# Kernel tuning notes

Measured on AMD Instinct MI355X. Metric: run time of the kernel, lower is better.

Reference implementation:

```python
import jax, jax.numpy as jnp
import numpy as np
from jax import lax

B, N, M = 4, 16384, 2048
C_IN = 64
RADII = (0.2, 0.4)
KS = (32, 64)
MLPS = ((64, 64, 128), (64, 96, 128))
EPS = 1e-5


def setup_inputs() -> dict:
    key = jax.random.key(0)
    ks = jax.random.split(key, 32)
    inp = {}
    inp["xyz"] = jax.random.uniform(ks[0], (B, 3, N), jnp.float32)
    inp["feature"] = jax.random.normal(ks[1], (B, C_IN, N), jnp.float32)
    ki = 2
    for s, chans in enumerate(MLPS):
        cin = C_IN + 3  # use_xyz concatenates relative xyz
        for l, cout in enumerate(chans):
            inp[f"w{s}{l}"] = jax.random.normal(ks[ki], (cout, cin), jnp.float32) * (1.0 / np.sqrt(cin)); ki += 1
            inp[f"g{s}{l}"] = jnp.ones((cout,), jnp.float32)
            inp[f"b{s}{l}"] = jnp.zeros((cout,), jnp.float32)
            cin = cout
    return inp


def _fps(points):
    """Farthest point sampling. points [N,3] -> [M] int32 indices (starts at 0)."""
    n = points.shape[0]
    def step(carry, _):
        dists, last = carry
        d = jnp.sum((points - points[last]) ** 2, axis=-1)
        dists = jnp.minimum(dists, d)
        nxt = jnp.argmax(dists).astype(jnp.int32)
        return (dists, nxt), nxt
    init = (jnp.full((n,), 1e10, jnp.float32), jnp.int32(0))
    _, rest = lax.scan(step, init, None, length=M - 1)
    return jnp.concatenate([jnp.zeros((1,), jnp.int32), rest])


def _ball_query(xyz, new_xyz, radius, k):
    """xyz [B,3,N], new_xyz [B,3,M] -> [B,M,k] int32. First-found semantics: empty
    slots are filled with the first valid index (pointnet2 ball_query behavior)."""
    xyz = lax.stop_gradient(xyz)
    new_xyz = lax.stop_gradient(new_xyz)
    n = xyz.shape[-1]
    sq_x = jnp.sum(xyz ** 2, axis=1)          # [B,N]
    sq_c = jnp.sum(new_xyz ** 2, axis=1)      # [B,M]
    d2 = sq_c[:, :, None] + sq_x[:, None, :] - 2.0 * jnp.einsum('bdm,bdn->bmn', new_xyz, xyz)
    scores = jnp.where(d2 < radius * radius, jnp.arange(n, dtype=jnp.int32), n)
    idx = -lax.top_k(-scores, k)[0]           # k smallest indices (in order)
    first = idx[..., :1]
    idx = jnp.where(idx >= n, first, idx)
    return jnp.where(idx >= n, 0, idx)


def _group(feat, idx):
    """feat [B,C,N], idx [B,M,K] -> [B,C,M,K]"""
    return jax.vmap(lambda f, i: f[:, i])(feat, idx)


def _forward(xyz, feature, params):
    idx = jax.vmap(_fps)(jnp.transpose(lax.stop_gradient(xyz), (0, 2, 1)))  # [B,M]
    new_xyz = jnp.take_along_axis(xyz, idx[:, None, :].astype(jnp.int32), axis=2)  # [B,3,M]
    feats = []
    for s in range(len(MLPS)):
        nidx = _ball_query(xyz, new_xyz, RADII[s], KS[s])        # [B,M,K]
        gxyz = _group(xyz, nidx) - new_xyz[..., None]            # [B,3,M,K]
        x = jnp.concatenate([gxyz, _group(feature, nidx)], axis=1)  # [B,3+C,M,K]
        for l in range(len(MLPS[s])):
            w = params[f"w{s}{l}"]; g = params[f"g{s}{l}"]; b = params[f"b{s}{l}"]
            x = jnp.einsum('oc,bcmk->bomk', w, x)                # 1x1 conv
            mu = jnp.mean(x, axis=(0, 2, 3), keepdims=True)      # train-mode BN
            var = jnp.mean((x - mu) ** 2, axis=(0, 2, 3), keepdims=True)
            x = (x - mu) * lax.rsqrt(var + EPS)
            x = x * g[None, :, None, None] + b[None, :, None, None]
            x = jax.nn.relu(x)
        feats.append(jnp.max(x, axis=3))                         # max over neighbors
    return new_xyz, jnp.concatenate(feats, axis=1)               # [B,3,M], [B,256,M]


def reference(xyz, feature, w00, g00, b00, w01, g01, b01, w02, g02, b02,
              w10, g10, b10, w11, g11, b11, w12, g12, b12):
    params = dict(w00=w00, g00=g00, b00=b00, w01=w01, g01=g01, b01=b01,
                  w02=w02, g02=g02, b02=b02, w10=w10, g10=g10, b10=b10,
                  w11=w11, g11=g11, b11=b11, w12=w12, g12=g12, b12=b12)
    return _forward(xyz, feature, params)
```

## Files before the change

kernel.cpp:

```cpp
#include <hip/hip_runtime.h>
#include <cstdint>

constexpr int B_ = 4, N_ = 16384, M_ = 2048;
constexpr int COLS0 = B_ * M_ * 32;
constexpr int COLS1 = B_ * M_ * 64;

constexpr int FPS_G   = 8;
constexpr int FPS_T   = 512;
constexpr int FPS_PPT = N_ / FPS_G / FPS_T;

constexpr size_t OFF_NEWXYZ = 0;
constexpr size_t OFF_NIDX0  = (size_t)B_ * 3 * M_ * 4;
constexpr size_t OFF_NIDX1  = OFF_NIDX0 + (size_t)COLS0 * 4;
constexpr size_t OFF_STATS  = OFF_NIDX1 + (size_t)COLS1 * 4;
constexpr size_t STATS_VALS = 64 * 2 * 128;
constexpr size_t OFF_COEF   = OFF_STATS + 6 * STATS_VALS * 8;
constexpr size_t OFF_SLOT   = OFF_COEF + 6 * 128 * 16;
constexpr size_t SLOT_BYTES = (size_t)B_ * 2 * FPS_G * 64;
constexpr size_t OFF_Z      = OFF_SLOT + SLOT_BYTES;
constexpr int ZSTRIDE = 96 * 64;

__global__ __launch_bounds__(FPS_T) void fps_kernel(const float* __restrict__ xyz,
                                                    float* __restrict__ newxyz,
                                                    float* __restrict__ outxyz,
                                                    unsigned long long* __restrict__ slots) {
#pragma clang fp contract(off)
  int bid = blockIdx.x;
  int b = bid >> 3, g = bid & 7;
  int t = threadIdx.x, lane = t & 63, wid = t >> 6;
  const float* xb = xyz + (size_t)b * 3 * N_;
  int nbase = g * (N_ / FPS_G) + t;
  float px[FPS_PPT], py[FPS_PPT], pz[FPS_PPT], dd[FPS_PPT];
#pragma unroll
  for (int j = 0; j < FPS_PPT; ++j) {
    int n = nbase + j * FPS_T;
    px[j] = xb[n]; py[j] = xb[N_ + n]; pz[j] = xb[2 * N_ + n];
    dd[j] = 1e10f;
    asm volatile("" : "+v"(px[j]), "+v"(py[j]), "+v"(pz[j]));
  }
  __shared__ unsigned long long s_red[2][FPS_T / 64];
  __shared__ unsigned long long s_win[2];
  size_t base = (size_t)b * 3 * M_;
  float fx = xb[0], fy = xb[N_], fz = xb[2 * N_];
  if (g == 0 && t == 0) {
    newxyz[base] = fx; newxyz[base + M_] = fy; newxyz[base + 2 * M_] = fz;
    outxyz[base] = fx; outxyz[base + M_] = fy; outxyz[base + 2 * M_] = fz;
  }
  unsigned long long* sb = slots + (size_t)b * 2 * FPS_G * 8;
  for (int s = 1; s < M_; ++s) {
    float bv = -1.f; int bi = 0;
#pragma unroll
    for (int j = 0; j < FPS_PPT; ++j) {
      float dx = px[j] - fx, dy = py[j] - fy, dz = pz[j] - fz;
      float d = (dx * dx + dy * dy) + dz * dz;
      float dm = dd[j];
      if (d < dm) dm = d;
      dd[j] = dm;
      if (dm > bv) { bv = dm; bi = nbase + j * FPS_T; }
    }
    unsigned long long key =
        ((unsigned long long)__float_as_uint(bv) << 32) |
        (unsigned)(((unsigned)s << 14) | (unsigned)(0x3FFF - bi));
#pragma unroll
    for (int off = 1; off < 64; off <<= 1) {
      unsigned long long o = __shfl_xor(key, off);
      if (o > key) key = o;
    }
    int p = s & 1;
    if (lane == 0) s_red[p][wid] = key;
    __syncthreads();
    if (wid == 0) {
      unsigned long long bk = s_red[p][lane & 7];
#pragma unroll
      for (int off = 1; off < 8; off <<= 1) {
        unsigned long long o = __shfl_xor(bk, off);
        if (o > bk) bk = o;
      }
      unsigned long long kk = 0;
      if (lane < FPS_G) {
        unsigned long long* sp = sb + ((size_t)p * FPS_G + lane) * 8;
        if (lane == g) atomicExch(sp, bk);
        unsigned long long v;
        unsigned tag = (unsigned)s;
        for (int it = 0; it < (1 << 18); ++it) {
          v = atomicAdd(sp, 0ull);
          if ((unsigned)((v >> 14) & 0x3FFFFull) == tag) break;
          __builtin_amdgcn_s_sleep(1);
        }
        kk = v;
      }
#pragma unroll
      for (int off = 1; off < 8; off <<= 1) {
        unsigned long long o = __shfl_xor(kk, off);
        if (o > kk) kk = o;
      }
      if (lane == 0) s_win[p] = kk;
    }
    __syncthreads();
    unsigned long long k = s_win[p];
    int w = 0x3FFF - (int)(k & 0x3FFFull);
    fx = xb[w]; fy = xb[N_ + w]; fz = xb[2 * N_ + w];
    if (g == 0 && t == 0) {
      newxyz[base + s] = fx; newxyz[base + M_ + s] = fy; newxyz[base + 2 * M_ + s] = fz;
      outxyz[base + s] = fx; outxyz[base + M_ + s] = fy; outxyz[base + 2 * M_ + s] = fz;
    }
  }
}

template <int KNB>
__global__ __launch_bounds__(256) void bq_kernel(const float* __restrict__ xyz,
                                                 const float* __restrict__ newxyz,
                                                 int* __restrict__ nidx, float r2) {
#pragma clang fp contract(off)
  int t = threadIdx.x, lane = t & 63, wq = t >> 6;
  int q = blockIdx.x * 4 + wq;
  int b = q >> 11, m = q & 2047;
  const float* xb = xyz + (size_t)b * 3 * N_;
  float cx = newxyz[((size_t)b * 3 + 0) * M_ + m];
  float cy = newxyz[((size_t)b * 3 + 1) * M_ + m];
  float cz = newxyz[((size_t)b * 3 + 2) * M_ + m];
  float sqc = (cx * cx + cy * cy) + cz * cz;
  int found = 0, first = 0;
  for (int c = 0; c < N_ / 64; ++c) {
    int n = c * 64 + lane;
    float x = xb[n], y = xb[N_ + n], z = xb[2 * N_ + n];
    float sqx = (x * x + y * y) + z * z;
    float dot = fmaf(cz, z, fmaf(cy, y, cx * x));
    float d2 = (sqc + sqx) - 2.0f * dot;
    bool in = d2 < r2;
    unsigned long long mask = __ballot(in);
    if (mask) {
      if (found == 0) first = c * 64 + (__ffsll((long long)mask) - 1);
      int pos = found + __popcll(mask & ((1ull << lane) - 1ull));
      if (in && pos < KNB) nidx[(size_t)q * KNB + pos] = n;
      found += __popcll(mask);
      if (found >= KNB) break;
    }
  }
  if (found < KNB) {
    int fill = (found == 0) ? 0 : first;
    for (int s = found + lane; s < KNB; s += 64) nidx[(size_t)q * KNB + s] = fill;
  }
}

__device__ __forceinline__ void stat_accum(float acc, int o, int cout, double* stats,
                                           int part, int lane) {
  float v1 = acc, v2 = acc * acc;
#pragma unroll
  for (int off = 1; off < 64; off <<= 1) {
    v1 += __shfl_xor(v1, off);
    v2 += __shfl_xor(v2, off);
  }
  if (lane == 0) {
    atomicAdd(stats + ((size_t)part * 2 + 0) * cout + o, (double)v1);
    atomicAdd(stats + ((size_t)part * 2 + 1) * cout + o, (double)v2);
  }
}

template <int KNB>
__global__ __launch_bounds__(256) void convL0_kernel(
    const float* __restrict__ w0,
    const float* __restrict__ xyz, const float* __restrict__ feat,
    const int* __restrict__ nidx, const float* __restrict__ newxyz,
    float* __restrict__ Z, double* __restrict__ stats) {
  int lane = threadIdx.x & 63, wq = threadIdx.x >> 6;
  int rec = blockIdx.x * 4 + wq;
  int col = rec * 64 + lane;
  float x[67];
  {
    int b = col / (M_ * KNB);
    int rem = col - b * (M_ * KNB);
    int m = rem / KNB;
    int n = nidx[col];
    const float* xb = xyz + (size_t)b * 3 * N_;
    x[0] = xb[n]          - newxyz[((size_t)b * 3 + 0) * M_ + m];
    x[1] = xb[N_ + n]     - newxyz[((size_t)b * 3 + 1) * M_ + m];
    x[2] = xb[2 * N_ + n] - newxyz[((size_t)b * 3 + 2) * M_ + m];
    const float* fb = feat + (size_t)b * 64 * N_;
#pragma unroll
    for (int c = 0; c < 64; ++c) x[3 + c] = fb[(size_t)c * N_ + n];
  }
  float* zr = Z + (size_t)rec * ZSTRIDE;
  int part = rec & 63;
  for (int o = 0; o < 64; ++o) {
    const float* wr = w0 + (size_t)o * 67;
    float acc = 0.f;
#pragma unroll
    for (int c = 0; c < 67; ++c) acc += wr[c] * x[c];
    zr[o * 64 + lane] = acc;
    stat_accum(acc, o, 64, stats, part, lane);
  }
}

template <int CIN, int COUT>
__global__ __launch_bounds__(256) void convMid_kernel(
    const float* __restrict__ w,
    const float4* __restrict__ coefIn,
    float* __restrict__ Z, double* __restrict__ stats) {
  int lane = threadIdx.x & 63, wq = threadIdx.x >> 6;
  int rec = blockIdx.x * 4 + wq;
  float* zr = Z + (size_t)rec * ZSTRIDE;
  float x[CIN];
#pragma unroll
  for (int c = 0; c < CIN; ++c) {
    float v = zr[c * 64 + lane];
    float4 cf = coefIn[c];
    x[c] = fmaxf(((v - cf.x) * cf.y) * cf.z + cf.w, 0.f);
  }
  int part = rec & 63;
  for (int o = 0; o < COUT; ++o) {
    const float* wr = w + (size_t)o * CIN;
    float acc = 0.f;
#pragma unroll
    for (int c = 0; c < CIN; ++c) acc += wr[c] * x[c];
    zr[o * 64 + lane] = acc;
    stat_accum(acc, o, COUT, stats, part, lane);
  }
}

template <int CIN>
__global__ __launch_bounds__(256) void convLastStats_kernel(
    const float* __restrict__ w, const float4* __restrict__ coefIn,
    const float* __restrict__ Z, double* __restrict__ stats) {
  int lane = threadIdx.x & 63, wq = threadIdx.x >> 6;
  int rec = blockIdx.x * 4 + wq;
  const float* zr = Z + (size_t)rec * ZSTRIDE;
  float x[CIN];
#pragma unroll
  for (int c = 0; c < CIN; ++c) {
    float v = zr[c * 64 + lane];
    float4 cf = coefIn[c];
    x[c] = fmaxf(((v - cf.x) * cf.y) * cf.z + cf.w, 0.f);
  }
  int part = rec & 63;
  for (int o = 0; o < 128; ++o) {
    const float* wr = w + (size_t)o * CIN;
    float acc = 0.f;
#pragma unroll
    for (int c = 0; c < CIN; ++c) acc += wr[c] * x[c];
    stat_accum(acc, o, 128, stats, part, lane);
  }
}

template <int CIN, int KNB>
__global__ __launch_bounds__(256) void convLastPool_kernel(
    const float* __restrict__ w, const float4* __restrict__ coefIn,
    const float4* __restrict__ coefOut,
    const float* __restrict__ Z, float* __restrict__ outFeats, int chBase) {
  int lane = threadIdx.x & 63, wq = threadIdx.x >> 6;
  int rec = blockIdx.x * 4 + wq;
  const float* zr = Z + (size_t)rec * ZSTRIDE;
  float x[CIN];
#pragma unroll
  for (int c = 0; c < CIN; ++c) {
    float v = zr[c * 64 + lane];
    float4 cf = coefIn[c];
    x[c] = fmaxf(((v - cf.x) * cf.y) * cf.z + cf.w, 0.f);
  }
  for (int o = 0; o < 128; ++o) {
    const float* wr = w + (size_t)o * CIN;
    float acc = 0.f;
#pragma unroll
    for (int c = 0; c < CIN; ++c) acc += wr[c] * x[c];
    float4 cf = coefOut[o];
    float z = fmaxf(((acc - cf.x) * cf.y) * cf.z + cf.w, 0.f);
    if (KNB == 64) {
#pragma unroll
      for (int off = 1; off < 64; off <<= 1) z = fmaxf(z, __shfl_xor(z, off));
      if (lane == 0) {
        int b = rec >> 11, m = rec & 2047;
        outFeats[((size_t)b * 256 + chBase + o) * M_ + m] = z;
      }
    } else {
#pragma unroll
      for (int off = 1; off < 32; off <<= 1) z = fmaxf(z, __shfl_xor(z, off));
      if ((lane & 31) == 0) {
        int grp = rec * 2 + (lane >> 5);
        int b = grp >> 11, m = grp & 2047;
        outFeats[((size_t)b * 256 + chBase + o) * M_ + m] = z;
      }
    }
  }
}

__global__ void coef_kernel(const double* __restrict__ stats, const float* __restrict__ g,
                            const float* __restrict__ bb, float4* __restrict__ coef,
                            int cout, double invcnt) {
  int ch = threadIdx.x;
  if (ch >= cout) return;
  double s1 = 0.0, s2 = 0.0;
  for (int p = 0; p < 64; ++p) {
    s1 += stats[((size_t)p * 2 + 0) * cout + ch];
    s2 += stats[((size_t)p * 2 + 1) * cout + ch];
  }
  double mean = s1 * invcnt;
  double var = s2 * invcnt - mean * mean;
  double rstd = 1.0 / sqrt(var + 1e-5);
  coef[ch] = make_float4((float)mean, (float)rstd, g[ch], bb[ch]);
}

extern "C" void kernel_launch(void* const* d_in, const int* in_sizes, int n_in,
                              void* d_out, int out_size, void* d_ws, size_t ws_size,
                              hipStream_t stream) {
  const float* xyz  = (const float*)d_in[0];
  const float* feat = (const float*)d_in[1];
  const float* w00 = (const float*)d_in[2],  *g00 = (const float*)d_in[3],  *b00 = (const float*)d_in[4];
  const float* w01 = (const float*)d_in[5],  *g01 = (const float*)d_in[6],  *b01 = (const float*)d_in[7];
  const float* w02 = (const float*)d_in[8],  *g02 = (const float*)d_in[9],  *b02 = (const float*)d_in[10];
  const float* w10 = (const float*)d_in[11], *g10 = (const float*)d_in[12], *b10 = (const float*)d_in[13];
  const float* w11 = (const float*)d_in[14], *g11 = (const float*)d_in[15], *b11 = (const float*)d_in[16];
  const float* w12 = (const float*)d_in[17], *g12 = (const float*)d_in[18], *b12 = (const float*)d_in[19];

  char* ws = (char*)d_ws;
  float*  newxyz = (float*)(ws + OFF_NEWXYZ);
  int*    nidx0  = (int*)(ws + OFF_NIDX0);
  int*    nidx1  = (int*)(ws + OFF_NIDX1);
  double* stats  = (double*)(ws + OFF_STATS);
  float4* coef   = (float4*)(ws + OFF_COEF);
  unsigned long long* slots = (unsigned long long*)(ws + OFF_SLOT);
  float*  Z      = (float*)(ws + OFF_Z);
  float* outF = (float*)d_out;
  float* outFeats = outF + (size_t)B_ * 3 * M_;

  hipMemsetAsync(ws + OFF_STATS, 0, 6 * STATS_VALS * 8, stream);
  hipMemsetAsync(ws + OFF_SLOT, 0, SLOT_BYTES, stream);
  fps_kernel<<<B_ * FPS_G, FPS_T, 0, stream>>>(xyz, newxyz, outF, slots);
  bq_kernel<32><<<(B_ * M_) / 4, 256, 0, stream>>>(xyz, newxyz, nidx0, (float)(0.2 * 0.2));
  bq_kernel<64><<<(B_ * M_) / 4, 256, 0, stream>>>(xyz, newxyz, nidx1, (float)(0.4 * 0.4));

  float4* c00 = coef + 0 * 128; float4* c01 = coef + 1 * 128; float4* c02 = coef + 2 * 128;
  float4* c10 = coef + 3 * 128; float4* c11 = coef + 4 * 128; float4* c12 = coef + 5 * 128;
  double* st0 = stats + 0 * STATS_VALS; double* st1 = stats + 1 * STATS_VALS;
  double* st2 = stats + 2 * STATS_VALS; double* st3 = stats + 3 * STATS_VALS;
  double* st4 = stats + 4 * STATS_VALS; double* st5 = stats + 5 * STATS_VALS;
  int gb0 = (COLS0 / 64) / 4, gb1 = (COLS1 / 64) / 4;

  convL0_kernel<32><<<gb0, 256, 0, stream>>>(w00, xyz, feat, nidx0, newxyz, Z, st0);
  coef_kernel<<<1, 128, 0, stream>>>(st0, g00, b00, c00, 64, 1.0 / COLS0);
  convMid_kernel<64, 64><<<gb0, 256, 0, stream>>>(w01, c00, Z, st1);
  coef_kernel<<<1, 128, 0, stream>>>(st1, g01, b01, c01, 64, 1.0 / COLS0);
  convLastStats_kernel<64><<<gb0, 256, 0, stream>>>(w02, c01, Z, st2);
  coef_kernel<<<1, 128, 0, stream>>>(st2, g02, b02, c02, 128, 1.0 / COLS0);
  convLastPool_kernel<64, 32><<<gb0, 256, 0, stream>>>(w02, c01, c02, Z, outFeats, 0);

  convL0_kernel<64><<<gb1, 256, 0, stream>>>(w10, xyz, feat, nidx1, newxyz, Z, st3);
  coef_kernel<<<1, 128, 0, stream>>>(st3, g10, b10, c10, 64, 1.0 / COLS1);
  convMid_kernel<64, 96><<<gb1, 256, 0, stream>>>(w11, c10, Z, st4);
  coef_kernel<<<1, 128, 0, stream>>>(st4, g11, b11, c11, 96, 1.0 / COLS1);
  convLastStats_kernel<96><<<gb1, 256, 0, stream>>>(w12, c11, Z, st5);
  coef_kernel<<<1, 128, 0, stream>>>(st5, g12, b12, c12, 128, 1.0 / COLS1);
  convLastPool_kernel<96, 64><<<gb1, 256, 0, stream>>>(w12, c11, c12, Z, outFeats, 128);
}
```

Measured before the change: 5.473 ms.

## Stage 64-column activation tiles in LDS and split output channels across waves

Each block now handles a single 64-column record. It stages the BN-ReLU'd input activations (or the gathered features for layer 0) into shared memory once. The four waves then split the output channels, each computing 8 channels at a time from the shared tile. This replaces the previous scheme where each wave held all CIN inputs in registers and swept every output channel serially. The goal is lower register pressure, higher occupancy and more ILP per wave, at the cost of LDS traffic, an extra barrier, and 4x more blocks.

```diff
diff --git a/kernel.cpp b/kernel.cpp
--- a/kernel.cpp
+++ b/kernel.cpp
@@ -157,64 +157,98 @@
   }
 }
 
+template <int CIN, int G>
+__device__ __forceinline__ void conv_sweep(const float* __restrict__ w, int o0,
+                                           const float* sx, int lane, float* acc) {
+#pragma unroll
+  for (int k = 0; k < G; ++k) acc[k] = 0.f;
+#pragma unroll 16
+  for (int c = 0; c < CIN; ++c) {
+    float xv = sx[c * 64 + lane];
+#pragma unroll
+    for (int k = 0; k < G; ++k) acc[k] += w[(size_t)(o0 + 4 * k) * CIN + c] * xv;
+  }
+}
+
+template <int CIN>
+__device__ __forceinline__ void stage_bn(const float* __restrict__ zr,
+                                         const float4* __restrict__ coefIn,
+                                         float* sx, int t) {
+  const float4* zr4 = (const float4*)zr;
+  float4* sx4 = (float4*)sx;
+  for (int e = t; e < CIN * 16; e += 256) {
+    int c = e >> 4;
+    float4 v = zr4[e];
+    float4 cf = coefIn[c];
+    float4 r;
+    r.x = fmaxf(((v.x - cf.x) * cf.y) * cf.z + cf.w, 0.f);
+    r.y = fmaxf(((v.y - cf.x) * cf.y) * cf.z + cf.w, 0.f);
+    r.z = fmaxf(((v.z - cf.x) * cf.y) * cf.z + cf.w, 0.f);
+    r.w = fmaxf(((v.w - cf.x) * cf.y) * cf.z + cf.w, 0.f);
+    sx4[e] = r;
+  }
+}
+
 template <int KNB>
 __global__ __launch_bounds__(256) void convL0_kernel(
-    const float* __restrict__ w0,
-    const float* __restrict__ xyz, const float* __restrict__ feat,
-    const int* __restrict__ nidx, const float* __restrict__ newxyz,
-    float* __restrict__ Z, double* __restrict__ stats) {
-  int lane = threadIdx.x & 63, wq = threadIdx.x >> 6;
-  int rec = blockIdx.x * 4 + wq;
-  int col = rec * 64 + lane;
-  float x[67];
-  {
+    const float* __restrict__ w0, const float* __restrict__ xyz,
+    const float* __restrict__ feat, const int* __restrict__ nidx,
+    const float* __restrict__ newxyz, float* __restrict__ Z, double* __restrict__ stats) {
+  __shared__ float sx[67 * 64];
+  __shared__ int snb[64];
+  int rec = blockIdx.x, t = threadIdx.x, lane = t & 63, wid = t >> 6;
+  if (t < 64) snb[t] = nidx[(size_t)rec * 64 + t];
+  __syncthreads();
+  for (int e = t; e < 67 * 64; e += 256) {
+    int c = e >> 6, l = e & 63;
+    int col = rec * 64 + l;
     int b = col / (M_ * KNB);
     int rem = col - b * (M_ * KNB);
     int m = rem / KNB;
-    int n = nidx[col];
-    const float* xb = xyz + (size_t)b * 3 * N_;
-    x[0] = xb[n]          - newxyz[((size_t)b * 3 + 0) * M_ + m];
-    x[1] = xb[N_ + n]     - newxyz[((size_t)b * 3 + 1) * M_ + m];
-    x[2] = xb[2 * N_ + n] - newxyz[((size_t)b * 3 + 2) * M_ + m];
-    const float* fb = feat + (size_t)b * 64 * N_;
-#pragma unroll
-    for (int c = 0; c < 64; ++c) x[3 + c] = fb[(size_t)c * N_ + n];
-  }
+    int n = snb[l];
+    float v;
+    if (c < 3) v = xyz[((size_t)b * 3 + c) * N_ + n] - newxyz[((size_t)b * 3 + c) * M_ + m];
+    else       v = feat[((size_t)b * 64 + (c - 3)) * N_ + n];
+    sx[e] = v;
+  }
+  __syncthreads();
   float* zr = Z + (size_t)rec * ZSTRIDE;
   int part = rec & 63;
-  for (int o = 0; o < 64; ++o) {
-    const float* wr = w0 + (size_t)o * 67;
-    float acc = 0.f;
-#pragma unroll
-    for (int c = 0; c < 67; ++c) acc += wr[c] * x[c];
-    zr[o * 64 + lane] = acc;
-    stat_accum(acc, o, 64, stats, part, lane);
+  float acc[8];
+#pragma unroll
+  for (int g = 0; g < 2; ++g) {
+    int o0 = wid + 32 * g;
+    conv_sweep<67, 8>(w0, o0, sx, lane, acc);
+#pragma unroll
+    for (int k = 0; k < 8; ++k) {
+      int o = o0 + 4 * k;
+      zr[o * 64 + lane] = acc[k];
+      stat_accum(acc[k], o, 64, stats, part, lane);
+    }
   }
 }
 
 template <int CIN, int COUT>
 __global__ __launch_bounds__(256) void convMid_kernel(
-    const float* __restrict__ w,
-    const float4* __restrict__ coefIn,
+    const float* __restrict__ w, const float4* __restrict__ coefIn,
     float* __restrict__ Z, double* __restrict__ stats) {
-  int lane = threadIdx.x & 63, wq = threadIdx.x >> 6;
-  int rec = blockIdx.x * 4 + wq;
+  __shared__ float sx[CIN * 64];
+  int rec = blockIdx.x, t = threadIdx.x, lane = t & 63, wid = t >> 6;
   float* zr = Z + (size_t)rec * ZSTRIDE;
-  float x[CIN];
-#pragma unroll
-  for (int c = 0; c < CIN; ++c) {
-    float v = zr[c * 64 + lane];
-    float4 cf = coefIn[c];
-    x[c] = fmaxf(((v - cf.x) * cf.y) * cf.z + cf.w, 0.f);
-  }
+  stage_bn<CIN>(zr, coefIn, sx, t);
+  __syncthreads();
   int part = rec & 63;
-  for (int o = 0; o < COUT; ++o) {
-    const float* wr = w + (size_t)o * CIN;
-    float acc = 0.f;
-#pragma unroll
-    for (int c = 0; c < CIN; ++c) acc += wr[c] * x[c];
-    zr[o * 64 + lane] = acc;
-    stat_accum(acc, o, COUT, stats, part, lane);
+  float acc[8];
+#pragma unroll
+  for (int g = 0; g < COUT / 32; ++g) {
+    int o0 = wid + 32 * g;
+    conv_sweep<CIN, 8>(w, o0, sx, lane, acc);
+#pragma unroll
+    for (int k = 0; k < 8; ++k) {
+      int o = o0 + 4 * k;
+      zr[o * 64 + lane] = acc[k];
+      stat_accum(acc[k], o, COUT, stats, part, lane);
+    }
   }
 }
 
@@ -222,23 +256,19 @@
 __global__ __launch_bounds__(256) void convLastStats_kernel(
     const float* __restrict__ w, const float4* __restrict__ coefIn,
     const float* __restrict__ Z, double* __restrict__ stats) {
-  int lane = threadIdx.x & 63, wq = threadIdx.x >> 6;
-  int rec = blockIdx.x * 4 + wq;
+  __shared__ float sx[CIN * 64];
+  int rec = blockIdx.x, t = threadIdx.x, lane = t & 63, wid = t >> 6;
   const float* zr = Z + (size_t)rec * ZSTRIDE;
-  float x[CIN];
-#pragma unroll
-  for (int c = 0; c < CIN; ++c) {
-    float v = zr[c * 64 + lane];
-    float4 cf = coefIn[c];
-    x[c] = fmaxf(((v - cf.x) * cf.y) * cf.z + cf.w, 0.f);
-  }
+  stage_bn<CIN>(zr, coefIn, sx, t);
+  __syncthreads();
   int part = rec & 63;
-  for (int o = 0; o < 128; ++o) {
-    const float* wr = w + (size_t)o * CIN;
-    float acc = 0.f;
-#pragma unroll
-    for (int c = 0; c < CIN; ++c) acc += wr[c] * x[c];
-    stat_accum(acc, o, 128, stats, part, lane);
+  float acc[8];
+#pragma unroll
+  for (int g = 0; g < 4; ++g) {
+    int o0 = wid + 32 * g;
+    conv_sweep<CIN, 8>(w, o0, sx, lane, acc);
+#pragma unroll
+    for (int k = 0; k < 8; ++k) stat_accum(acc[k], o0 + 4 * k, 128, stats, part, lane);
   }
 }
 
@@ -247,37 +277,36 @@
     const float* __restrict__ w, const float4* __restrict__ coefIn,
     const float4* __restrict__ coefOut,
     const float* __restrict__ Z, float* __restrict__ outFeats, int chBase) {
-  int lane = threadIdx.x & 63, wq = threadIdx.x >> 6;
-  int rec = blockIdx.x * 4 + wq;
+  __shared__ float sx[CIN * 64];
+  int rec = blockIdx.x, t = threadIdx.x, lane = t & 63, wid = t >> 6;
   const float* zr = Z + (size_t)rec * ZSTRIDE;
-  float x[CIN];
-#pragma unroll
-  for (int c = 0; c < CIN; ++c) {
-    float v = zr[c * 64 + lane];
-    float4 cf = coefIn[c];
-    x[c] = fmaxf(((v - cf.x) * cf.y) * cf.z + cf.w, 0.f);
-  }
-  for (int o = 0; o < 128; ++o) {
-    const float* wr = w + (size_t)o * CIN;
-    float acc = 0.f;
-#pragma unroll
-    for (int c = 0; c < CIN; ++c) acc += wr[c] * x[c];
-    float4 cf = coefOut[o];
-    float z = fmaxf(((acc - cf.x) * cf.y) * cf.z + cf.w, 0.f);
-    if (KNB == 64) {
-#pragma unroll
-      for (int off = 1; off < 64; off <<= 1) z = fmaxf(z, __shfl_xor(z, off));
-      if (lane == 0) {
-        int b = rec >> 11, m = rec & 2047;
-        outFeats[((size_t)b * 256 + chBase + o) * M_ + m] = z;
-      }
-    } else {
-#pragma unroll
-      for (int off = 1; off < 32; off <<= 1) z = fmaxf(z, __shfl_xor(z, off));
-      if ((lane & 31) == 0) {
-        int grp = rec * 2 + (lane >> 5);
-        int b = grp >> 11, m = grp & 2047;
-        outFeats[((size_t)b * 256 + chBase + o) * M_ + m] = z;
+  stage_bn<CIN>(zr, coefIn, sx, t);
+  __syncthreads();
+  float acc[8];
+#pragma unroll
+  for (int g = 0; g < 4; ++g) {
+    int o0 = wid + 32 * g;
+    conv_sweep<CIN, 8>(w, o0, sx, lane, acc);
+#pragma unroll
+    for (int k = 0; k < 8; ++k) {
+      int o = o0 + 4 * k;
+      float4 cf = coefOut[o];
+      float z = fmaxf(((acc[k] - cf.x) * cf.y) * cf.z + cf.w, 0.f);
+      if (KNB == 64) {
+#pragma unroll
+        for (int off = 1; off < 64; off <<= 1) z = fmaxf(z, __shfl_xor(z, off));
+        if (lane == 0) {
+          int b = rec >> 11, m = rec & 2047;
+          outFeats[((size_t)b * 256 + chBase + o) * M_ + m] = z;
+        }
+      } else {
+#pragma unroll
+        for (int off = 1; off < 32; off <<= 1) z = fmaxf(z, __shfl_xor(z, off));
+        if ((lane & 31) == 0) {
+          int grp = rec * 2 + (lane >> 5);
+          int b = grp >> 11, m = grp & 2047;
+          outFeats[((size_t)b * 256 + chBase + o) * M_ + m] = z;
+        }
       }
     }
   }
@@ -333,7 +362,7 @@
   double* st0 = stats + 0 * STATS_VALS; double* st1 = stats + 1 * STATS_VALS;
   double* st2 = stats + 2 * STATS_VALS; double* st3 = stats + 3 * STATS_VALS;
   double* st4 = stats + 4 * STATS_VALS; double* st5 = stats + 5 * STATS_VALS;
-  int gb0 = (COLS0 / 64) / 4, gb1 = (COLS1 / 64) / 4;
+  int gb0 = COLS0 / 64, gb1 = COLS1 / 64;
 
   convL0_kernel<32><<<gb0, 256, 0, stream>>>(w00, xyz, feat, nidx0, newxyz, Z, st0);
   coef_kernel<<<1, 128, 0, stream>>>(st0, g00, b00, c00, 64, 1.0 / COLS0);
```

New measurement: 7.636 ms. 39.5% more time.
